# Kernel tuning notes

Hardware: AMD Instinct MI355X
Metric: run time of the kernel (lower is better)

The kernel has to match this reference:

```python
import jax, jax.numpy as jnp
import numpy as np
from jax import lax

# Dimensions (see shape_source)
B, J, I, E, H = 256, 128, 64, 512, 512   # batch, target len, source len, embed, hidden
MAXJW = 128                               # max jump width
WJ = 2 * MAXJW + 1                        # size of jump-width set (257)
ALPHA_P0 = 1.0
EPS = 1e-29


def setup_inputs() -> dict:
    key = jax.random.key(0)
    ks = jax.random.split(key, 10)
    return {
        "y_hidden": jax.random.normal(ks[0], (B, J, E), jnp.float32),
        "y_hidden_null": jax.random.normal(ks[1], (1, 1, E), jnp.float32),
        "W_trans": jax.random.normal(ks[2], (E, H), jnp.float32) * 0.02,
        "b_trans": jnp.zeros((H,), jnp.float32),
        "W_jump": jax.random.normal(ks[3], (H, WJ), jnp.float32) * 0.02,
        "b_jump": jnp.zeros((WJ,), jnp.float32),
        "W_p0": jax.random.normal(ks[4], (H, 1), jnp.float32) * 0.02,
        "b_p0": jnp.zeros((1,), jnp.float32),
        # emission probs p(source_t | target_state_k), kept near 1 to avoid
        # underflow of the unrescaled HMM forward product (as in original).
        "emission": jax.random.uniform(ks[5], (B, 2 * J, I), jnp.float32) * 0.5 + 0.75,
        "source_lengths": jax.random.randint(ks[6], (B,), 1, I + 1, dtype=jnp.int32),
        "target_lengths": jax.random.randint(ks[7], (B,), 1, J + 1, dtype=jnp.int32),
    }


def _build_transition(y_hidden, y_hidden_null, W_trans, b_trans, W_jump, b_jump, W_p0, b_p0):
    # get_transition: Dense(tanh) -> Dense(softmax) jump widths; Dense(sigmoid) p0.
    ts = jnp.tanh(y_hidden @ W_trans + b_trans)           # [B,J,H]
    ts_null = jnp.tanh(y_hidden_null @ W_trans + b_trans) # [1,1,H]
    jump_prob = jax.nn.softmax(ts @ W_jump + b_jump, axis=-1)  # [B,J,WJ]
    p0_scalar = ALPHA_P0 * jax.nn.sigmoid(ts_null @ W_p0 + b_p0)[0, 0, 0]
    p0 = jnp.broadcast_to(p0_scalar, (y_hidden.shape[0], J))  # tile to [B,J]
    # gather jump widths: row i takes jump_prob[:, i, MAXJW + k - i] for k in [0,J)
    idx = MAXJW + jnp.arange(J)[None, :] - jnp.arange(J)[:, None]        # [J,J]
    idxb = jnp.broadcast_to(idx[None], (jump_prob.shape[0], J, J))
    jw = jnp.take_along_axis(jump_prob, idxb, axis=2)                    # [B,J,J]
    jw = jw * (1.0 - p0[:, :, None]) / jnp.sum(jw, axis=2, keepdims=True)
    diag_p0 = p0[:, :, None] * jnp.eye(J, dtype=jw.dtype)                # [B,J,J]
    T_half = jnp.concatenate([jw, diag_p0], axis=2)                      # [B,J,2J]
    return jnp.concatenate([T_half, T_half], axis=1)                     # [B,2J,2J]


def reference(y_hidden, y_hidden_null, W_trans, b_trans, W_jump, b_jump,
              W_p0, b_p0, emission, source_lengths, target_lengths):
    T = _build_transition(y_hidden, y_hidden_null, W_trans, b_trans,
                          W_jump, b_jump, W_p0, b_p0)       # [B,2J,2J]
    e = jnp.transpose(emission, (2, 0, 1))                  # [I,B,2J]
    # tf.scan with no initializer: f_0 = emission at source position 0
    f0 = e[0]

    def step(f, et):
        f_next = jnp.einsum('bj,bjk->bk', f, T) * et        # forward recursion
        return f_next, f_next

    _, fs = lax.scan(step, f0, e[1:])
    fs = jnp.concatenate([f0[None], fs], axis=0)            # [I,B,2J]
    fbt = jnp.transpose(fs, (1, 2, 0))                      # [B,2J,I]
    last_idx = (source_lengths - 1).astype(jnp.int32)[:, None, None]
    last = jnp.take_along_axis(fbt, last_idx, axis=2)[:, :, 0]  # [B,2J]
    m = (jnp.arange(J)[None, :] < target_lengths[:, None]).astype(last.dtype)
    mask = jnp.concatenate([m, m], axis=1)                  # [B,2J]
    return jnp.log(jnp.sum(last * mask, axis=1) + EPS)      # [B]
```

## Files before the change

### kernel.cpp

```cpp
#include <hip/hip_runtime.h>
#include <stdint.h>

typedef __attribute__((ext_vector_type(8))) short bf16x8;
typedef __attribute__((ext_vector_type(4))) float f32x4;

__device__ __forceinline__ unsigned short f2bf(float f) {
  union { float f; unsigned int u; } un; un.f = f;
  unsigned int r = un.u + 0x7fffu + ((un.u >> 16) & 1u);
  return (unsigned short)(r >> 16);
}

__device__ __forceinline__ float bf2f(unsigned short u) {
  union { unsigned int u; float f; } un; un.u = ((unsigned int)u) << 16;
  return un.f;
}

__device__ __forceinline__ float tanh_fast(float x) {
  x = fminf(15.f, fmaxf(-15.f, x));
  float e = __expf(2.f * x);
  return (e - 1.f) / (e + 1.f);
}

__device__ __forceinline__ unsigned int cvt_pk_bf16(float lo, float hi) {
  unsigned int r;
  asm("v_cvt_pk_bf16_f32 %0, %1, %2" : "=v"(r) : "v"(lo), "v"(hi));
  return r;
}

__device__ __forceinline__ void gload_lds16(const void* g, void* l) {
  __builtin_amdgcn_global_load_lds(
      (const __attribute__((address_space(1))) unsigned int*)(unsigned long long)g,
      (__attribute__((address_space(3))) unsigned int*)(unsigned int)(unsigned long long)l,
      16, 0, 0);
}

__global__ __launch_bounds__(256) void cvt_weights_p0(
    const float* __restrict__ Wt_in, const float* __restrict__ Wj_in,
    const float* __restrict__ ynull, const float* __restrict__ b_trans,
    const float* __restrict__ W_p0, const float* __restrict__ b_p0,
    unsigned short* __restrict__ wt, unsigned short* __restrict__ wj,
    float* __restrict__ p0buf) {
  if (blockIdx.x < 1536) {
    const int i = blockIdx.x * 256 + threadIdx.x;
    if (i < 512 * 512) {
      const int c = i >> 9, r = i & 511;
      wt[i] = f2bf(Wt_in[(size_t)r * 512 + c]);
    } else {
      const int j = i - 512 * 512;
      const int c = j >> 9, r = j & 511;
      wj[j] = f2bf(Wj_in[(size_t)r * 257 + c]);
    }
    return;
  }
  __shared__ float red[256];
  const int hh = threadIdx.x;
  float a0 = 0.f, a1 = 0.f;
  for (int e = 0; e < 512; ++e) {
    const float y = ynull[e];
    a0 = fmaf(y, Wt_in[(size_t)e * 512 + hh], a0);
    a1 = fmaf(y, Wt_in[(size_t)e * 512 + hh + 256], a1);
  }
  red[hh] = tanhf(a0 + b_trans[hh]) * W_p0[hh] +
            tanhf(a1 + b_trans[hh + 256]) * W_p0[hh + 256];
  __syncthreads();
  for (int s = 128; s > 0; s >>= 1) {
    if (hh < s) red[hh] += red[hh + s];
    __syncthreads();
  }
  if (hh == 0) {
    const float z = red[0] + b_p0[0];
    const float p0 = 1.f / (1.f + __expf(-z));
    p0buf[0] = p0;
    p0buf[1] = 1.f - p0;
  }
}


__global__ __launch_bounds__(256, 2) void gemm_af32(
    const float* __restrict__ A, const unsigned short* __restrict__ Bt,
    const float* __restrict__ bias, unsigned short* __restrict__ Cout,
    int M, int N, int K) {
  __shared__ unsigned short sA[128 * 32];
  __shared__ unsigned short sB[128 * 32];
  const int tid = threadIdx.x;
  const int lane = tid & 63;
  const int wave = tid >> 6;
  const int wr = wave >> 1, wc = wave & 1;
  const int m0 = blockIdx.x * 128, n0 = blockIdx.y * 128;

  f32x4 acc[4][4] = {};

  const int srow = lane >> 2;
  const int sl = lane & 3;
  const int scol = sl * 8;
  const int wsz = (srow >> 1) & 3;
  const int scolw = (sl ^ wsz) * 8;
  const int c0 = wave * 2, c1 = wave * 2 + 1;
  const float* Af0 = A + (size_t)(m0 + c0 * 16 + srow) * K + scol;
  const float* Af1 = A + (size_t)(m0 + c1 * 16 + srow) * K + scol;
  const unsigned short* Br0 = Bt + (size_t)(n0 + c0 * 16 + srow) * K + scolw;
  const unsigned short* Br1 = Bt + (size_t)(n0 + c1 * 16 + srow) * K + scolw;

  float4 a00 = *reinterpret_cast<const float4*>(Af0);
  float4 a01 = *reinterpret_cast<const float4*>(Af0 + 4);
  float4 a10 = *reinterpret_cast<const float4*>(Af1);
  float4 a11 = *reinterpret_cast<const float4*>(Af1 + 4);

  const int r15 = lane & 15;
  const int oslot = ((lane >> 4) ^ ((r15 >> 1) & 3)) * 8;

  for (int kk = 0; kk < K; kk += 32) {
    __syncthreads();
    {
      union { unsigned int u[4]; bf16x8 v; } p;
      p.u[0] = cvt_pk_bf16(a00.x, a00.y);
      p.u[1] = cvt_pk_bf16(a00.z, a00.w);
      p.u[2] = cvt_pk_bf16(a01.x, a01.y);
      p.u[3] = cvt_pk_bf16(a01.z, a01.w);
      *reinterpret_cast<bf16x8*>(&sA[c0 * 512 + srow * 32 + scolw]) = p.v;
      p.u[0] = cvt_pk_bf16(a10.x, a10.y);
      p.u[1] = cvt_pk_bf16(a10.z, a10.w);
      p.u[2] = cvt_pk_bf16(a11.x, a11.y);
      p.u[3] = cvt_pk_bf16(a11.z, a11.w);
      *reinterpret_cast<bf16x8*>(&sA[c1 * 512 + srow * 32 + scolw]) = p.v;
    }
    gload_lds16(Br0 + kk, &sB[c0 * 512]);
    gload_lds16(Br1 + kk, &sB[c1 * 512]);
    __syncthreads();
    if (kk + 32 < K) {
      a00 = *reinterpret_cast<const float4*>(Af0 + kk + 32);
      a01 = *reinterpret_cast<const float4*>(Af0 + kk + 36);
      a10 = *reinterpret_cast<const float4*>(Af1 + kk + 32);
      a11 = *reinterpret_cast<const float4*>(Af1 + kk + 36);
    }
    bf16x8 af[4], bfr[4];
#pragma unroll
    for (int mi = 0; mi < 4; ++mi)
      af[mi] = *reinterpret_cast<const bf16x8*>(
          &sA[(wr * 64 + mi * 16 + r15) * 32 + oslot]);
#pragma unroll
    for (int ni = 0; ni < 4; ++ni)
      bfr[ni] = *reinterpret_cast<const bf16x8*>(
          &sB[(wc * 64 + ni * 16 + r15) * 32 + oslot]);
#pragma unroll
    for (int mi = 0; mi < 4; ++mi)
#pragma unroll
      for (int ni = 0; ni < 4; ++ni)
        acc[mi][ni] = __builtin_amdgcn_mfma_f32_16x16x32_bf16(
            af[mi], bfr[ni], acc[mi][ni], 0, 0, 0);
  }

  const int crow0 = m0 + wr * 64 + (lane >> 4) * 4;
  const int ccol0 = n0 + wc * 64 + r15;
#pragma unroll
  for (int mi = 0; mi < 4; ++mi) {
#pragma unroll
    for (int ni = 0; ni < 4; ++ni) {
      const int gcol = ccol0 + ni * 16;
      const float bv = bias[gcol];
#pragma unroll
      for (int r = 0; r < 4; ++r) {
        const int grow = crow0 + mi * 16 + r;
        Cout[(size_t)grow * N + gcol] = f2bf(tanh_fast(acc[mi][ni][r] + bv));
      }
    }
  }
}

__global__ __launch_bounds__(256, 2) void gemm_tt(
    const unsigned short* __restrict__ A, const unsigned short* __restrict__ Bt,
    const float* __restrict__ bias, unsigned short* __restrict__ Cout,
    int M, int N, int K) {
  __shared__ unsigned short sA[2][128 * 32];
  __shared__ unsigned short sB[2][128 * 32];
  const int tid = threadIdx.x;
  const int lane = tid & 63;
  const int wave = tid >> 6;
  const int wr = wave >> 1, wc = wave & 1;
  const int id = blockIdx.x;
  const int xcd = id & 7, qq = id >> 3;
  const int m0 = (xcd * 32 + (qq >> 1)) * 128;
  const int n0 = (qq & 1) * 128;

  f32x4 acc[4][4] = {};

  const int srow = lane >> 2;
  const int sl = lane & 3;
  const int wsz = (srow >> 1) & 3;
  const int scolw = (sl ^ wsz) * 8;
  const int c0 = wave * 2, c1 = wave * 2 + 1;
  const unsigned short* Ar0 = A + (size_t)(m0 + c0 * 16 + srow) * K + scolw;
  const unsigned short* Ar1 = A + (size_t)(m0 + c1 * 16 + srow) * K + scolw;
  const unsigned short* Br0 = Bt + (size_t)(n0 + c0 * 16 + srow) * K + scolw;
  const unsigned short* Br1 = Bt + (size_t)(n0 + c1 * 16 + srow) * K + scolw;

  const int r15 = lane & 15;
  const int oslot = ((lane >> 4) ^ ((r15 >> 1) & 3)) * 8;
  const int nt = K >> 5;

  auto stage = [&](int bi, int t) {
    gload_lds16(Ar0 + t * 32, &sA[bi][c0 * 512]);
    gload_lds16(Ar1 + t * 32, &sA[bi][c1 * 512]);
    gload_lds16(Br0 + t * 32, &sB[bi][c0 * 512]);
    gload_lds16(Br1 + t * 32, &sB[bi][c1 * 512]);
  };

  stage(0, 0);
  __syncthreads();
  for (int t = 0; t < nt; ++t) {
    if (t + 1 < nt) stage((t + 1) & 1, t + 1);
    bf16x8 af[4], bfr[4];
#pragma unroll
    for (int mi = 0; mi < 4; ++mi)
      af[mi] = *reinterpret_cast<const bf16x8*>(
          &sA[t & 1][(wr * 64 + mi * 16 + r15) * 32 + oslot]);
#pragma unroll
    for (int ni = 0; ni < 4; ++ni)
      bfr[ni] = *reinterpret_cast<const bf16x8*>(
          &sB[t & 1][(wc * 64 + ni * 16 + r15) * 32 + oslot]);
#pragma unroll
    for (int mi = 0; mi < 4; ++mi)
#pragma unroll
      for (int ni = 0; ni < 4; ++ni)
        acc[mi][ni] = __builtin_amdgcn_mfma_f32_16x16x32_bf16(
            af[mi], bfr[ni], acc[mi][ni], 0, 0, 0);
    __syncthreads();
  }

  const int crow0 = m0 + wr * 64 + (lane >> 4) * 4;
  const int ccol0 = n0 + wc * 64 + r15;
#pragma unroll
  for (int mi = 0; mi < 4; ++mi) {
#pragma unroll
    for (int ni = 0; ni < 4; ++ni) {
      const int gcol = ccol0 + ni * 16;
      const float bv = bias[gcol];
#pragma unroll
      for (int r = 0; r < 4; ++r) {
        const int grow = crow0 + mi * 16 + r;
        Cout[(size_t)grow * N + gcol] = f2bf(acc[mi][ni][r] + bv);
      }
    }
  }
}

__global__ __launch_bounds__(256) void wsoftmax_kernel(
    const unsigned short* __restrict__ logits, const float* __restrict__ p0buf,
    unsigned short* __restrict__ jwout) {
  const int lane = threadIdx.x & 63;
  const int wave = threadIdx.x >> 6;
  const int row = blockIdx.x * 4 + wave;
  const int i = row & 127;
  const unsigned short* lrow = logits + (size_t)row * 256 + (128 - i);
  const float v0 = bf2f(lrow[lane]);
  const float v1 = bf2f(lrow[lane + 64]);
  float mx = fmaxf(v0, v1);
#pragma unroll
  for (int off = 32; off > 0; off >>= 1) mx = fmaxf(mx, __shfl_xor(mx, off));
  const float e0 = __expf(v0 - mx);
  const float e1 = __expf(v1 - mx);
  float s = e0 + e1;
#pragma unroll
  for (int off = 32; off > 0; off >>= 1) s += __shfl_xor(s, off);
  const float scale = p0buf[1] / s;
  unsigned short* orow = jwout + (size_t)row * 128;
  orow[lane] = f2bf(e0 * scale);
  orow[lane + 64] = f2bf(e1 * scale);
}

#define SE_STRIDE 264
__global__ __launch_bounds__(256, 1) void forward_fused(
    const unsigned short* __restrict__ jwb,
    const float* __restrict__ emission,
    const float* __restrict__ p0buf, const int* __restrict__ slen_p,
    const int* __restrict__ tlen_p, float* __restrict__ out) {
  __shared__ __align__(16) float se[64 * SE_STRIDE];
  __shared__ __align__(16) unsigned short gl16[128];
  const int b = blockIdx.x;
  const int tid = threadIdx.x;
  const float* eb = emission + (size_t)b * 16384;

  bf16x8 bfr[4][8];
  const int l = tid & 63;
  const int m = l & 15;
  const int q = l >> 4;

  if (tid >= 64) {
#pragma unroll
    for (int it = 0; it < 6; ++it) {
      const int tau = (tid - 64) + 192 * it;
      if (tau < 1024) {
        const int t0 = (tau & 15) * 4;
        const int mm = (tau >> 4) & 15;
        const int nt0 = ((tau >> 8) & 1) * 4;
        const int half = (tau >> 9) & 1;
        const int kbase = half * 128 + nt0 * 16 + mm;
        const float4 v0 = *reinterpret_cast<const float4*>(&eb[(size_t)(kbase) * 64 + t0]);
        const float4 v1 = *reinterpret_cast<const float4*>(&eb[(size_t)(kbase + 16) * 64 + t0]);
        const float4 v2 = *reinterpret_cast<const float4*>(&eb[(size_t)(kbase + 32) * 64 + t0]);
        const float4 v3 = *reinterpret_cast<const float4*>(&eb[(size_t)(kbase + 48) * 64 + t0]);
        const int jinv0 = half * 128 + mm * 8 + nt0;
        float* d = &se[(size_t)t0 * SE_STRIDE + jinv0];
        *reinterpret_cast<float4*>(d) = (float4){v0.x, v1.x, v2.x, v3.x};
        *reinterpret_cast<float4*>(d + SE_STRIDE) = (float4){v0.y, v1.y, v2.y, v3.y};
        *reinterpret_cast<float4*>(d + 2 * SE_STRIDE) = (float4){v0.z, v1.z, v2.z, v3.z};
        *reinterpret_cast<float4*>(d + 3 * SE_STRIDE) = (float4){v0.w, v1.w, v2.w, v3.w};
      }
    }
  } else {
    const unsigned short* jwt = jwb + (size_t)b * 16384;
#pragma unroll
    for (int kt = 0; kt < 4; ++kt) {
      const int r0 = kt * 32 + q * 8;
#pragma unroll
      for (int nt = 0; nt < 8; ++nt) {
        const int c = nt * 16 + m;
        bf16x8 v;
#pragma unroll
        for (int j = 0; j < 8; ++j) v[j] = (short)jwt[(size_t)(r0 + j) * 128 + c];
        bfr[kt][nt] = v;
      }
    }
  }
  __syncthreads();
  if (tid >= 64) return;

  const float p0 = p0buf[0];
  const int S = slen_p[b];
  const int T = tlen_p[b];

  float gown[8];
  {
    const float4 i0a = *reinterpret_cast<const float4*>(&se[m * 8]);
    const float4 i0b = *reinterpret_cast<const float4*>(&se[m * 8 + 4]);
    const float4 i1a = *reinterpret_cast<const float4*>(&se[128 + m * 8]);
    const float4 i1b = *reinterpret_cast<const float4*>(&se[128 + m * 8 + 4]);
    gown[0] = i0a.x + i1a.x; gown[1] = i0a.y + i1a.y;
    gown[2] = i0a.z + i1a.z; gown[3] = i0a.w + i1a.w;
    gown[4] = i0b.x + i1b.x; gown[5] = i0b.y + i1b.y;
    gown[6] = i0b.z + i1b.z; gown[7] = i0b.w + i1b.w;
  }
  gl16[(2 * q) * 16 + m]     = f2bf(gown[2 * q]);
  gl16[(2 * q + 1) * 16 + m] = f2bf(gown[2 * q + 1]);

  for (int t = 1; t < S; ++t) {
    const float* st = &se[(size_t)t * SE_STRIDE];
    const float4 pe0a = *reinterpret_cast<const float4*>(&st[m * 8]);
    const float4 pe0b = *reinterpret_cast<const float4*>(&st[m * 8 + 4]);
    const float4 pe1a = *reinterpret_cast<const float4*>(&st[128 + m * 8]);
    const float4 pe1b = *reinterpret_cast<const float4*>(&st[128 + m * 8 + 4]);
    const float e0[8] = {pe0a.x, pe0a.y, pe0a.z, pe0a.w, pe0b.x, pe0b.y, pe0b.z, pe0b.w};
    const float e1[8] = {pe1a.x, pe1a.y, pe1a.z, pe1a.w, pe1b.x, pe1b.y, pe1b.z, pe1b.w};
    float h[8];
#pragma unroll
    for (int nt = 0; nt < 8; ++nt) h[nt] = gown[nt] * (p0 * e1[nt]);
    bf16x8 af[4];
#pragma unroll
    for (int kt = 0; kt < 4; ++kt)
      af[kt] = *reinterpret_cast<const bf16x8*>(&gl16[kt * 32 + q * 8]);
    f32x4 acc[8];
#pragma unroll
    for (int nt = 0; nt < 8; ++nt) {
      f32x4 a = __builtin_amdgcn_mfma_f32_16x16x32_bf16(
          af[0], bfr[0][nt], (f32x4){0.f, 0.f, 0.f, 0.f}, 0, 0, 0);
      a = __builtin_amdgcn_mfma_f32_16x16x32_bf16(af[1], bfr[1][nt], a, 0, 0, 0);
      a = __builtin_amdgcn_mfma_f32_16x16x32_bf16(af[2], bfr[2][nt], a, 0, 0, 0);
      acc[nt] = __builtin_amdgcn_mfma_f32_16x16x32_bf16(af[3], bfr[3][nt], a, 0, 0, 0);
    }
#pragma unroll
    for (int nt = 0; nt < 8; ++nt) gown[nt] = fmaf(acc[nt][0], e0[nt], h[nt]);
    gl16[(2 * q) * 16 + m]     = f2bf(gown[2 * q]);
    gl16[(2 * q + 1) * 16 + m] = f2bf(gown[2 * q + 1]);
  }

  float val = 0.f;
#pragma unroll
  for (int nt = 0; nt < 8; ++nt)
    if (nt * 16 + m < T) val += gown[nt];
#pragma unroll
  for (int off = 1; off < 16; off <<= 1) val += __shfl_xor(val, off);
  if (l == 0) out[b] = logf(val + 1e-29f);
}

extern "C" void kernel_launch(void* const* d_in, const int* in_sizes, int n_in,
                              void* d_out, int out_size, void* d_ws, size_t ws_size,
                              hipStream_t stream) {
  const float* y_hidden = (const float*)d_in[0];
  const float* y_null   = (const float*)d_in[1];
  const float* W_trans  = (const float*)d_in[2];
  const float* b_trans  = (const float*)d_in[3];
  const float* W_jump   = (const float*)d_in[4];
  const float* b_jump   = (const float*)d_in[5];
  const float* W_p0     = (const float*)d_in[6];
  const float* b_p0     = (const float*)d_in[7];
  const float* emission = (const float*)d_in[8];
  const int* slen = (const int*)d_in[9];
  const int* tlen = (const int*)d_in[10];
  float* out = (float*)d_out;

  char* ws = (char*)d_ws;
  unsigned short* ts16  = (unsigned short*)ws;
  unsigned short* lg16  = (unsigned short*)(ws + 33554432);
  unsigned short* wt16t = (unsigned short*)(ws + 50331648);
  unsigned short* wj16t = (unsigned short*)(ws + 50855936);
  float* p0buf          = (float*)(ws + 51118080);
  unsigned short* jwb16 = (unsigned short*)(ws + 51118336);

  cvt_weights_p0<<<dim3(1537), dim3(256), 0, stream>>>(
      W_trans, W_jump, y_null, b_trans, W_p0, b_p0, wt16t, wj16t, p0buf);

  gemm_af32<<<dim3(256, 4), dim3(256), 0, stream>>>(y_hidden, wt16t, b_trans, ts16,
                                                    32768, 512, 512);
  gemm_tt<<<dim3(512), dim3(256), 0, stream>>>(ts16, wj16t, b_jump, lg16,
                                               32768, 256, 512);
  wsoftmax_kernel<<<dim3(8192), dim3(256), 0, stream>>>(lg16, p0buf, jwb16);
  forward_fused<<<dim3(256), dim3(256), 0, stream>>>(jwb16, emission, p0buf,
                                                     slen, tlen, out);
}
```

Measured before the change: 116.4 us.

## Fuse jump-logit GEMM with windowed softmax in shared memory

Merges the second GEMM (ts @ W_jump) and the windowed softmax into one kernel. Each block computes a 64x256 logit tile, stages it in LDS as fp32, and performs the shifted-window softmax and bf16 packing there. This removes the 16 MB bf16 logits round-trip through global memory and one kernel launch. In exchange, tiles become 64x256 (16 accumulators per wave), and the 66 KB LDS footprint may limit occupancy to one block per CU.

```diff
diff --git a/kernel.cpp b/kernel.cpp
--- a/kernel.cpp
+++ b/kernel.cpp
@@ -8,11 +8,6 @@
   union { float f; unsigned int u; } un; un.f = f;
   unsigned int r = un.u + 0x7fffu + ((un.u >> 16) & 1u);
   return (unsigned short)(r >> 16);
-}
-
-__device__ __forceinline__ float bf2f(unsigned short u) {
-  union { unsigned int u; float f; } un; un.u = ((unsigned int)u) << 16;
-  return un.f;
 }
 
 __device__ __forceinline__ float tanh_fast(float x) {
@@ -167,105 +162,109 @@
   }
 }
 
-__global__ __launch_bounds__(256, 2) void gemm_tt(
-    const unsigned short* __restrict__ A, const unsigned short* __restrict__ Bt,
-    const float* __restrict__ bias, unsigned short* __restrict__ Cout,
-    int M, int N, int K) {
-  __shared__ unsigned short sA[2][128 * 32];
-  __shared__ unsigned short sB[2][128 * 32];
+#define LG_STRIDE 260
+__global__ __launch_bounds__(256, 2) void gemm2_sm(
+    const unsigned short* __restrict__ A,
+    const unsigned short* __restrict__ Bt,
+    const float* __restrict__ bias,
+    const float* __restrict__ p0buf,
+    unsigned short* __restrict__ jwout) {
+  __shared__ __align__(16) char smem[64 * LG_STRIDE * 4];
   const int tid = threadIdx.x;
   const int lane = tid & 63;
   const int wave = tid >> 6;
+  const int m0 = blockIdx.x * 64;
+  const int r15 = lane & 15;
+  const int q = lane >> 4;
   const int wr = wave >> 1, wc = wave & 1;
-  const int id = blockIdx.x;
-  const int xcd = id & 7, qq = id >> 3;
-  const int m0 = (xcd * 32 + (qq >> 1)) * 128;
-  const int n0 = (qq & 1) * 128;
-
-  f32x4 acc[4][4] = {};
+
+  f32x4 acc[2][8] = {};
 
   const int srow = lane >> 2;
   const int sl = lane & 3;
-  const int wsz = (srow >> 1) & 3;
-  const int scolw = (sl ^ wsz) * 8;
-  const int c0 = wave * 2, c1 = wave * 2 + 1;
-  const unsigned short* Ar0 = A + (size_t)(m0 + c0 * 16 + srow) * K + scolw;
-  const unsigned short* Ar1 = A + (size_t)(m0 + c1 * 16 + srow) * K + scolw;
-  const unsigned short* Br0 = Bt + (size_t)(n0 + c0 * 16 + srow) * K + scolw;
-  const unsigned short* Br1 = Bt + (size_t)(n0 + c1 * 16 + srow) * K + scolw;
-
-  const int r15 = lane & 15;
-  const int oslot = ((lane >> 4) ^ ((r15 >> 1) & 3)) * 8;
-  const int nt = K >> 5;
+  const int scolw = ((sl ^ ((srow >> 1) & 3))) * 8;
+  const int oslot = ((q ^ ((r15 >> 1) & 3))) * 8;
 
   auto stage = [&](int bi, int t) {
-    gload_lds16(Ar0 + t * 32, &sA[bi][c0 * 512]);
-    gload_lds16(Ar1 + t * 32, &sA[bi][c1 * 512]);
-    gload_lds16(Br0 + t * 32, &sB[bi][c0 * 512]);
-    gload_lds16(Br1 + t * 32, &sB[bi][c1 * 512]);
+    unsigned short* base = (unsigned short*)(smem + bi * 20480);
+#pragma unroll
+    for (int cc = 0; cc < 5; ++cc) {
+      const int chunk = wave + cc * 4;
+      if (chunk < 4) {
+        gload_lds16(A + (size_t)(m0 + chunk * 16 + srow) * 512 + t * 32 + scolw,
+                    base + chunk * 512);
+      } else {
+        gload_lds16(Bt + (size_t)((chunk - 4) * 16 + srow) * 512 + t * 32 + scolw,
+                    base + 2048 + (chunk - 4) * 512);
+      }
+    }
+  };
+  auto compute = [&](int bi) {
+    const unsigned short* base = (const unsigned short*)(smem + bi * 20480);
+    bf16x8 af[2], bfr[8];
+#pragma unroll
+    for (int mi = 0; mi < 2; ++mi)
+      af[mi] = *reinterpret_cast<const bf16x8*>(
+          &base[(wr * 32 + mi * 16 + r15) * 32 + oslot]);
+#pragma unroll
+    for (int ni = 0; ni < 8; ++ni)
+      bfr[ni] = *reinterpret_cast<const bf16x8*>(
+          &base[2048 + (wc * 128 + ni * 16 + r15) * 32 + oslot]);
+#pragma unroll
+    for (int mi = 0; mi < 2; ++mi)
+#pragma unroll
+      for (int ni = 0; ni < 8; ++ni)
+        acc[mi][ni] = __builtin_amdgcn_mfma_f32_16x16x32_bf16(
+            af[mi], bfr[ni], acc[mi][ni], 0, 0, 0);
   };
 
   stage(0, 0);
   __syncthreads();
-  for (int t = 0; t < nt; ++t) {
-    if (t + 1 < nt) stage((t + 1) & 1, t + 1);
-    bf16x8 af[4], bfr[4];
-#pragma unroll
-    for (int mi = 0; mi < 4; ++mi)
-      af[mi] = *reinterpret_cast<const bf16x8*>(
-          &sA[t & 1][(wr * 64 + mi * 16 + r15) * 32 + oslot]);
-#pragma unroll
-    for (int ni = 0; ni < 4; ++ni)
-      bfr[ni] = *reinterpret_cast<const bf16x8*>(
-          &sB[t & 1][(wc * 64 + ni * 16 + r15) * 32 + oslot]);
-#pragma unroll
-    for (int mi = 0; mi < 4; ++mi)
-#pragma unroll
-      for (int ni = 0; ni < 4; ++ni)
-        acc[mi][ni] = __builtin_amdgcn_mfma_f32_16x16x32_bf16(
-            af[mi], bfr[ni], acc[mi][ni], 0, 0, 0);
+  for (int t = 0; t < 16; ++t) {
+    if (t + 1 < 16) stage((t + 1) & 1, t + 1);
+    compute(t & 1);
     __syncthreads();
   }
 
-  const int crow0 = m0 + wr * 64 + (lane >> 4) * 4;
-  const int ccol0 = n0 + wc * 64 + r15;
-#pragma unroll
-  for (int mi = 0; mi < 4; ++mi) {
-#pragma unroll
-    for (int ni = 0; ni < 4; ++ni) {
-      const int gcol = ccol0 + ni * 16;
-      const float bv = bias[gcol];
+  float* lg = (float*)smem;
+#pragma unroll
+  for (int mi = 0; mi < 2; ++mi) {
+#pragma unroll
+    for (int ni = 0; ni < 8; ++ni) {
+      const int col = wc * 128 + ni * 16 + r15;
+      const float bv = bias[col];
 #pragma unroll
       for (int r = 0; r < 4; ++r) {
-        const int grow = crow0 + mi * 16 + r;
-        Cout[(size_t)grow * N + gcol] = f2bf(acc[mi][ni][r] + bv);
+        const int rowL = wr * 32 + mi * 16 + q * 4 + r;
+        lg[rowL * LG_STRIDE + col] = acc[mi][ni][r] + bv;
       }
     }
   }
-}
-
-__global__ __launch_bounds__(256) void wsoftmax_kernel(
-    const unsigned short* __restrict__ logits, const float* __restrict__ p0buf,
-    unsigned short* __restrict__ jwout) {
-  const int lane = threadIdx.x & 63;
-  const int wave = threadIdx.x >> 6;
-  const int row = blockIdx.x * 4 + wave;
-  const int i = row & 127;
-  const unsigned short* lrow = logits + (size_t)row * 256 + (128 - i);
-  const float v0 = bf2f(lrow[lane]);
-  const float v1 = bf2f(lrow[lane + 64]);
-  float mx = fmaxf(v0, v1);
-#pragma unroll
-  for (int off = 32; off > 0; off >>= 1) mx = fmaxf(mx, __shfl_xor(mx, off));
-  const float e0 = __expf(v0 - mx);
-  const float e1 = __expf(v1 - mx);
-  float s = e0 + e1;
-#pragma unroll
-  for (int off = 32; off > 0; off >>= 1) s += __shfl_xor(s, off);
+  __syncthreads();
+
+  const int rowL = tid >> 2, p = tid & 3;
+  const int grow = m0 + rowL;
+  const int i = grow & 127;
+  float* lrow = lg + rowL * LG_STRIDE + (128 - i) + p * 32;
+  float mx = -1e30f;
+#pragma unroll
+  for (int j = 0; j < 32; ++j) mx = fmaxf(mx, lrow[j]);
+  mx = fmaxf(mx, __shfl_xor(mx, 1));
+  mx = fmaxf(mx, __shfl_xor(mx, 2));
+  float s = 0.f;
+#pragma unroll
+  for (int j = 0; j < 32; ++j) {
+    const float e = __expf(lrow[j] - mx);
+    lrow[j] = e;
+    s += e;
+  }
+  s += __shfl_xor(s, 1);
+  s += __shfl_xor(s, 2);
   const float scale = p0buf[1] / s;
-  unsigned short* orow = jwout + (size_t)row * 128;
-  orow[lane] = f2bf(e0 * scale);
-  orow[lane + 64] = f2bf(e1 * scale);
+  unsigned int* orow = (unsigned int*)(jwout + (size_t)grow * 128 + p * 32);
+#pragma unroll
+  for (int j = 0; j < 16; ++j)
+    orow[j] = cvt_pk_bf16(lrow[2 * j] * scale, lrow[2 * j + 1] * scale);
 }
 
 #define SE_STRIDE 264
@@ -400,7 +399,6 @@
 
   char* ws = (char*)d_ws;
   unsigned short* ts16  = (unsigned short*)ws;
-  unsigned short* lg16  = (unsigned short*)(ws + 33554432);
   unsigned short* wt16t = (unsigned short*)(ws + 50331648);
   unsigned short* wj16t = (unsigned short*)(ws + 50855936);
   float* p0buf          = (float*)(ws + 51118080);
@@ -411,9 +409,7 @@
 
   gemm_af32<<<dim3(256, 4), dim3(256), 0, stream>>>(y_hidden, wt16t, b_trans, ts16,
                                                     32768, 512, 512);
-  gemm_tt<<<dim3(512), dim3(256), 0, stream>>>(ts16, wj16t, b_jump, lg16,
-                                               32768, 256, 512);
-  wsoftmax_kernel<<<dim3(8192), dim3(256), 0, stream>>>(lg16, p0buf, jwb16);
+  gemm2_sm<<<dim3(512), dim3(256), 0, stream>>>(ts16, wj16t, b_jump, p0buf, jwb16);
   forward_fused<<<dim3(256), dim3(256), 0, stream>>>(jwb16, emission, p0buf,
                                                      slen, tlen, out);
 }
```

New measurement: 113.5 us. 2.5% less time.
